# Optimization experiments

Hardware: AMD Instinct MI355X
Metric: run time of the kernel (lower is better)

## Reference

```python
import jax, jax.numpy as jnp
import numpy as np

DIM = 256
RADIUS = 3
DIAM = 2 * RADIUS + 1          # 7
NNEIGH = DIAM * DIAM           # 49
B, H, W = 2, 64, 64
EPS_LN = 1e-6
EPS_NORM = 1e-7


def conv1x1(x, w, b):
    # x: [B,Cin,H,W], w: [Cout,Cin], b: [Cout]
    return jnp.einsum('oi,bihw->bohw', w, x) + b[None, :, None, None]


def layernorm2d(x, g, b):
    # channel-wise norm as in LayerNorm2d (mean/var over channel dim)
    u = x.mean(1, keepdims=True)
    s = ((x - u) ** 2).mean(1, keepdims=True)
    xn = (x - u) / jnp.sqrt(s + EPS_LN)
    return g[None, :, None, None] * xn + b[None, :, None, None]


def unfold_reflect(x, r):
    # torch F.unfold(pad(x, reflect, r), kernel=2r+1).reshape(B,C,D*D,H,W)
    d = 2 * r + 1
    hh, ww = x.shape[2], x.shape[3]
    xp = jnp.pad(x, ((0, 0), (0, 0), (r, r), (r, r)), mode='reflect')
    pats = [xp[:, :, i:i + hh, j:j + ww] for i in range(d) for j in range(d)]
    return jnp.stack(pats, axis=2)  # [B,C,D*D,H,W]


def setup_inputs() -> dict:
    key = jax.random.key(0)
    ks = jax.random.split(key, 20)
    sc_c = 1.0 / np.sqrt(DIM)
    sc_f = 1.0 / np.sqrt(NNEIGH + DIM)
    inp = {
        'spatial_feats': jax.random.normal(ks[0], (B, DIM, H, W), jnp.float32),
        'semantic_feats': jax.random.normal(ks[1], (B, DIM, H, W), jnp.float32),
        # range_proj: conv1x1 -> LN2d -> SiLU -> conv1x1
        'rp_w1': jax.random.normal(ks[2], (DIM, DIM), jnp.float32) * sc_c,
        'rp_b1': jnp.zeros((DIM,), jnp.float32),
        'rp_g': jnp.ones((DIM,), jnp.float32),
        'rp_be': jnp.zeros((DIM,), jnp.float32),
        'rp_w2': jax.random.normal(ks[3], (DIM, DIM), jnp.float32) * sc_c,
        'rp_b2': jnp.zeros((DIM,), jnp.float32),
        # fixup_proj: conv1x1(49+C->49) -> LN2d -> SiLU -> conv1x1(49->49)
        'fp_w1': jax.random.normal(ks[4], (NNEIGH, NNEIGH + DIM), jnp.float32) * sc_f,
        'fp_b1': jnp.zeros((NNEIGH,), jnp.float32),
        'fp_g': jnp.ones((NNEIGH,), jnp.float32),
        'fp_be': jnp.zeros((NNEIGH,), jnp.float32),
        'fp_w2': jax.random.normal(ks[5], (NNEIGH, NNEIGH), jnp.float32) * (1.0 / np.sqrt(NNEIGH)),
        'fp_b2': jnp.zeros((NNEIGH,), jnp.float32),
        # output_proj: conv1x1 -> LN2d -> conv1x1
        'op_w1': jax.random.normal(ks[6], (DIM, DIM), jnp.float32) * sc_c,
        'op_b1': jnp.zeros((DIM,), jnp.float32),
        'op_g': jnp.ones((DIM,), jnp.float32),
        'op_be': jnp.zeros((DIM,), jnp.float32),
        'op_w2': jax.random.normal(ks[7], (DIM, DIM), jnp.float32) * sc_c,
        'op_b2': jnp.zeros((DIM,), jnp.float32),
        'sigma_spatial': jnp.ones((), jnp.float32),
    }
    return inp


def reference(spatial_feats, semantic_feats,
              rp_w1, rp_b1, rp_g, rp_be, rp_w2, rp_b2,
              fp_w1, fp_b1, fp_g, fp_be, fp_w2, fp_b2,
              op_w1, op_b1, op_g, op_be, op_w2, op_b2,
              sigma_spatial):
    scale = jnp.asarray(DIM ** 0.5, spatial_feats.dtype)
    # range_proj(semantic_feats)
    px = conv1x1(semantic_feats, rp_w1, rp_b1)
    px = jax.nn.silu(layernorm2d(px, rp_g, rp_be))
    px = conv1x1(px, rp_w2, rp_b2)  # [B,C,H,W]

    # spatial (Gaussian) kernel over the window
    lin = jnp.linspace(-1.0, 1.0, DIAM)
    xg, yg = jnp.meshgrid(lin, lin, indexing='ij')
    spatial_kernel = jnp.exp(-(xg ** 2 + yg ** 2) / (2.0 * sigma_spatial ** 2))
    spatial_kernel = spatial_kernel.reshape(1, NNEIGH, 1, 1)

    # range kernel: local similarity + softmax over the 49 neighbors
    queries = unfold_reflect(px, RADIUS)                       # [B,C,N,H,W]
    sim = jnp.einsum('bcnhw,bchw->bnhw', queries, px) / scale
    range_kernel = jax.nn.softmax(sim.astype(jnp.float32), axis=1).astype(px.dtype)

    # neighborhoods of spatial features
    neighborhoods = unfold_reflect(spatial_feats, RADIUS)      # [B,C,N,H,W]

    # gated fixup correction
    ck = range_kernel * spatial_kernel                          # [B,N,H,W]
    fx = conv1x1(jnp.concatenate([ck, semantic_feats], axis=1), fp_w1, fp_b1)
    fx = jax.nn.silu(layernorm2d(fx, fp_g, fp_be))
    fx = conv1x1(fx, fp_w2, fp_b2)
    ck = ck + ck * jax.nn.sigmoid(fx)
    ck = ck / (ck.sum(1, keepdims=True) + EPS_NORM)

    # weighted neighborhood sum
    out = jnp.einsum('bcnhw,bnhw->bchw', neighborhoods, ck)

    # output_proj (note: no SiLU here, matching the module)
    out = conv1x1(out, op_w1, op_b1)
    out = layernorm2d(out, op_g, op_be)
    out = conv1x1(out, op_w2, op_b2)
    return out
```

## Files before the change

### kernel.cpp

```cpp
#include <hip/hip_runtime.h>
#include <cstdint>

#define HW 4096
#define C_ 256
#define NN 49
#define KW 305

typedef __bf16 bf16;
typedef bf16 bf16x8 __attribute__((ext_vector_type(8)));
typedef bf16 bf16x4 __attribute__((ext_vector_type(4)));
typedef bf16 bf16x2 __attribute__((ext_vector_type(2)));
typedef float f32x4 __attribute__((ext_vector_type(4)));

#define GLD16(src, dst) __builtin_amdgcn_global_load_lds( \
    (const __attribute__((address_space(1))) uint32_t*)(src), \
    (__attribute__((address_space(3))) uint32_t*)(dst), 16, 0, 0)

__device__ __forceinline__ int refl(int i) { return i < 0 ? -i : (i > 63 ? 126 - i : i); }
__device__ __forceinline__ float sigmoidf_(float x) { return 1.f / (1.f + __expf(-x)); }

__global__ __launch_bounds__(256) void setup_k(const float* __restrict__ spatial,
                                               const float* __restrict__ semantic,
                                               const float* __restrict__ rp_w1,
                                               const float* __restrict__ rp_w2,
                                               const float* __restrict__ op_w1,
                                               const float* __restrict__ op_w2,
                                               const float* __restrict__ fp_w1,
                                               const float* __restrict__ fp_w2,
                                               const float* __restrict__ sigma,
                                               bf16* __restrict__ spb, bf16* __restrict__ seb,
                                               bf16* __restrict__ wrp1, bf16* __restrict__ wrp2,
                                               bf16* __restrict__ wop1, bf16* __restrict__ wop2,
                                               bf16* __restrict__ w1ckb, bf16* __restrict__ w1sb,
                                               bf16* __restrict__ w2Tg, float* __restrict__ sk)
{
    __shared__ float tile[32][33];
    const int bid = blockIdx.x, t = threadIdx.x;
    if (bid < 4096) {
        int z = bid >> 10, r = bid & 1023;
        int b = z & 1;
        const float* src = (z >> 1) ? semantic : spatial;
        bf16* dst = (z >> 1) ? seb : spb;
        int p0 = (r & 127) * 32, c0 = (r >> 7) * 32;
        int tx = t & 31, ty = t >> 5;
        const float* s = src + (size_t)b * C_ * HW;
        #pragma unroll
        for (int i = 0; i < 32; i += 8)
            tile[ty + i][tx] = s[(size_t)(c0 + ty + i) * HW + p0 + tx];
        __syncthreads();
        int p = t >> 3, cq = (t & 7) * 4;
        bf16x4 o = {(bf16)tile[cq][p], (bf16)tile[cq + 1][p], (bf16)tile[cq + 2][p], (bf16)tile[cq + 3][p]};
        *(bf16x4*)&dst[((size_t)b * HW + p0 + p) * C_ + c0 + cq] = o;
        return;
    }
    int pid = bid - 4096;
    if (pid < 256) {
        const float* src = (pid < 64) ? rp_w1 : (pid < 128) ? rp_w2 : (pid < 192) ? op_w1 : op_w2;
        bf16* dst = (pid < 64) ? wrp1 : (pid < 128) ? wrp2 : (pid < 192) ? wop1 : wop2;
        int i = ((pid & 63) * 256 + t) * 4;
        f32x4 v = *(const f32x4*)&src[i];
        bf16x4 o = {(bf16)v[0], (bf16)v[1], (bf16)v[2], (bf16)v[3]};
        *(bf16x4*)&dst[i] = o;
    } else if (pid == 256) {
        if (t < NN) {
            int i = t / 7, j = t % 7;
            float xg = (i - 3) * (1.f / 3.f), yg = (j - 3) * (1.f / 3.f);
            float s = sigma[0];
            sk[t] = __expf(-(xg * xg + yg * yg) / (2.f * s * s));
        }
    } else if (pid < 270) {
        int idx = (pid - 257) * 256 + t;
        if (idx < NN * 64) {
            int k = idx >> 6, o = idx & 63;
            w1ckb[idx] = (o < NN) ? (bf16)fp_w1[o * KW + k] : (bf16)0.f;
        }
    } else if (pid < 334) {
        int idx = (pid - 270) * 256 + t;
        int o = idx >> 8, c = idx & 255;
        w1sb[idx] = (o < NN) ? (bf16)fp_w1[o * KW + NN + c] : (bf16)0.f;
    } else {
        int idx = (pid - 334) * 256 + t;
        if (idx < NN * 64) {
            int k = idx >> 6, o = idx & 63;
            w2Tg[idx] = (o < NN) ? (bf16)fp_w2[o * NN + k] : (bf16)0.f;
        }
    }
}

__device__ __forceinline__ void stage_b(const bf16* __restrict__ Wp, bf16* dst, int kc, int t)
{
    const bf16* gB = Wp + (size_t)(t >> 2) * C_ + kc + (((t & 3) ^ ((t >> 3) & 3)) * 8);
    #pragma unroll
    for (int ii = 0; ii < 4; ++ii)
        GLD16(gB + (size_t)ii * 64 * C_, dst + ii * 2048 + t * 8);
}

template<bool SILU, int MODE>
__global__ __launch_bounds__(256) void conv_pair(const bf16* __restrict__ X,
                                                 const bf16* __restrict__ W1,
                                                 const float* __restrict__ b1v,
                                                 const float* __restrict__ g,
                                                 const float* __restrict__ be,
                                                 const bf16* __restrict__ W2,
                                                 const float* __restrict__ b2v,
                                                 void* __restrict__ Yv)
{
    __shared__ __align__(16) bf16 Xf[32 * 256];
    __shared__ __align__(16) bf16 Mid[32 * 256];
    __shared__ __align__(16) bf16 Bs[2][256 * 32];
    __shared__ float lnred[32][4][2];
    const int t = threadIdx.x;
    const int lane = t & 63, wc = t >> 6;
    const int l15 = lane & 15, kb = lane >> 4;
    const long q0 = (long)blockIdx.x * 32;

    {
        const int r8 = t >> 5, slot = t & 31;
        const bf16* gX = X + (q0 + r8) * C_ + ((slot ^ (r8 & 7)) * 8);
        #pragma unroll
        for (int i = 0; i < 4; ++i)
            GLD16(gX + (size_t)i * 8 * C_, &Xf[i * 2048 + t * 8]);
    }
    stage_b(W1, &Bs[0][0], 0, t);

    const int x7 = l15 & 7;
    const int bsl = (kb ^ ((l15 >> 1) & 3)) * 8;
    int boff[4];
    #pragma unroll
    for (int n = 0; n < 4; ++n)
        boff[n] = (wc * 64 + n * 16 + l15) * 32 + bsl;
    const int a0base = l15 * 256;
    const int a1base = (16 + l15) * 256;

    f32x4 acc[2][4];
    #pragma unroll
    for (int m = 0; m < 2; ++m)
        #pragma unroll
        for (int n = 0; n < 4; ++n) acc[m][n] = (f32x4){0.f, 0.f, 0.f, 0.f};

    __syncthreads();
    int cur = 0;
    #pragma unroll
    for (int ks = 0; ks < 8; ++ks) {
        if (ks < 7) stage_b(W1, &Bs[cur ^ 1][0], (ks + 1) * 32, t);
        const int ko = ((ks * 4 + kb) ^ x7) * 8;
        bf16x8 a0 = *(const bf16x8*)&Xf[a0base + ko];
        bf16x8 a1 = *(const bf16x8*)&Xf[a1base + ko];
        #pragma unroll
        for (int n = 0; n < 4; ++n) {
            bf16x8 b = *(const bf16x8*)&Bs[cur][boff[n]];
            acc[0][n] = __builtin_amdgcn_mfma_f32_16x16x32_bf16(a0, b, acc[0][n], 0, 0, 0);
            acc[1][n] = __builtin_amdgcn_mfma_f32_16x16x32_bf16(a1, b, acc[1][n], 0, 0, 0);
        }
        __syncthreads();
        cur ^= 1;
    }

    stage_b(W2, &Bs[0][0], 0, t);

    float s4[2][4], ss4[2][4];
    #pragma unroll
    for (int m = 0; m < 2; ++m)
        #pragma unroll
        for (int r = 0; r < 4; ++r) { s4[m][r] = 0.f; ss4[m][r] = 0.f; }
    #pragma unroll
    for (int n = 0; n < 4; ++n) {
        float bo = b1v[wc * 64 + n * 16 + l15];
        #pragma unroll
        for (int m = 0; m < 2; ++m)
            #pragma unroll
            for (int r = 0; r < 4; ++r) {
                float v = acc[m][n][r] + bo;
                acc[m][n][r] = v;
                s4[m][r] += v; ss4[m][r] += v * v;
            }
    }
    #pragma unroll
    for (int off = 1; off <= 8; off <<= 1)
        #pragma unroll
        for (int m = 0; m < 2; ++m)
            #pragma unroll
            for (int r = 0; r < 4; ++r) {
                s4[m][r]  += __shfl_xor(s4[m][r], off, 64);
                ss4[m][r] += __shfl_xor(ss4[m][r], off, 64);
            }
    if (l15 == 0) {
        #pragma unroll
        for (int m = 0; m < 2; ++m)
            #pragma unroll
            for (int r = 0; r < 4; ++r) {
                lnred[m * 16 + kb * 4 + r][wc][0] = s4[m][r];
                lnred[m * 16 + kb * 4 + r][wc][1] = ss4[m][r];
            }
    }
    __syncthreads();
    float mean[2][4], rstd[2][4];
    #pragma unroll
    for (int m = 0; m < 2; ++m)
        #pragma unroll
        for (int r = 0; r < 4; ++r) {
            int p = m * 16 + kb * 4 + r;
            float st  = lnred[p][0][0] + lnred[p][1][0] + lnred[p][2][0] + lnred[p][3][0];
            float sst = lnred[p][0][1] + lnred[p][1][1] + lnred[p][2][1] + lnred[p][3][1];
            mean[m][r] = st * (1.f / 256.f);
            float var = sst * (1.f / 256.f) - mean[m][r] * mean[m][r];
            rstd[m][r] = rsqrtf(var + 1e-6f);
        }
    #pragma unroll
    for (int n = 0; n < 4; ++n) {
        int ch = wc * 64 + n * 16 + l15;
        float gv = g[ch], bev = be[ch];
        #pragma unroll
        for (int m = 0; m < 2; ++m)
            #pragma unroll
            for (int r = 0; r < 4; ++r) {
                float y = (acc[m][n][r] - mean[m][r]) * rstd[m][r] * gv + bev;
                if (SILU) y *= sigmoidf_(y);
                int p = m * 16 + kb * 4 + r;
                Mid[p * 256 + (((ch >> 3) ^ (p & 7)) * 8) + (ch & 7)] = (bf16)y;
            }
    }
    __syncthreads();

    f32x4 acc2[2][4];
    #pragma unroll
    for (int m = 0; m < 2; ++m)
        #pragma unroll
        for (int n = 0; n < 4; ++n) acc2[m][n] = (f32x4){0.f, 0.f, 0.f, 0.f};
    cur = 0;
    #pragma unroll
    for (int ks = 0; ks < 8; ++ks) {
        if (ks < 7) stage_b(W2, &Bs[cur ^ 1][0], (ks + 1) * 32, t);
        const int ko = ((ks * 4 + kb) ^ x7) * 8;
        bf16x8 a0 = *(const bf16x8*)&Mid[a0base + ko];
        bf16x8 a1 = *(const bf16x8*)&Mid[a1base + ko];
        #pragma unroll
        for (int n = 0; n < 4; ++n) {
            bf16x8 b = *(const bf16x8*)&Bs[cur][boff[n]];
            acc2[0][n] = __builtin_amdgcn_mfma_f32_16x16x32_bf16(a0, b, acc2[0][n], 0, 0, 0);
            acc2[1][n] = __builtin_amdgcn_mfma_f32_16x16x32_bf16(a1, b, acc2[1][n], 0, 0, 0);
        }
        __syncthreads();
        cur ^= 1;
    }

    if constexpr (MODE == 0) {
        #pragma unroll
        for (int n = 0; n < 4; ++n) {
            int ch = wc * 64 + n * 16 + l15;
            float bo = b2v[ch];
            #pragma unroll
            for (int m = 0; m < 2; ++m)
                #pragma unroll
                for (int r = 0; r < 4; ++r)
                    Xf[(m * 16 + kb * 4 + r) * 256 + ch] = (bf16)(acc2[m][n][r] + bo);
        }
        __syncthreads();
        bf16* Y = (bf16*)Yv;
        const int p = t >> 3, cb = (t & 7) * 32;
        #pragma unroll
        for (int i = 0; i < 4; ++i) {
            bf16x8 v = *(const bf16x8*)&Xf[p * 256 + cb + i * 8];
            *(bf16x8*)&Y[(q0 + p) * C_ + cb + i * 8] = v;
        }
    } else {
        float* Y = (float*)Yv;
        const int bb = (int)(q0 >> 12);
        #pragma unroll
        for (int n = 0; n < 4; ++n) {
            int ch = wc * 64 + n * 16 + l15;
            float bo = b2v[ch];
            #pragma unroll
            for (int m = 0; m < 2; ++m) {
                int pp = (int)(q0 & 4095) + m * 16 + kb * 4;
                f32x4 val = {acc2[m][n][0] + bo, acc2[m][n][1] + bo,
                             acc2[m][n][2] + bo, acc2[m][n][3] + bo};
                *(f32x4*)&Y[((size_t)bb * C_ + ch) * HW + pp] = val;
            }
        }
    }
}

__global__ __launch_bounds__(256) void attn_k(const bf16* __restrict__ px,
                                              const bf16* __restrict__ spb,
                                              const bf16* __restrict__ seb,
                                              const bf16* __restrict__ w1sb,
                                              const bf16* __restrict__ w1ckb,
                                              const bf16* __restrict__ w2Tg,
                                              const float* __restrict__ b1,
                                              const float* __restrict__ b2,
                                              const float* __restrict__ g,
                                              const float* __restrict__ be,
                                              const float* __restrict__ sk,
                                              bf16* __restrict__ outb)
{
    __shared__ __align__(16) bf16 uni[100 * 256];
    __shared__ float S[112 * 17];
    __shared__ float fxs[64 * 17];
    __shared__ __align__(16) bf16 w2lT[NN * 64];
    __shared__ __align__(16) bf16 w1lT[NN * 64];
    __shared__ float ckl[16][64];
    __shared__ float hb[4][64];

    const int t = threadIdx.x, lane = t & 63, wid = t >> 6;
    const int l15 = lane & 15, kb = lane >> 4;
    const int blk = blockIdx.x;
    const int batch = blk >> 8, tt = blk & 255;
    const int h0 = (tt >> 4) * 4, w0 = (tt & 15) * 4;
    const long base = (long)batch * HW;

    const float bo  = (lane < NN) ? b1[lane] : 0.f;
    const float gl  = (lane < NN) ? g[lane] : 0.f;
    const float bel = (lane < NN) ? be[lane] : 0.f;
    const float b2l = (lane < NN) ? b2[lane] : 0.f;
    const float skv = (lane < NN) ? sk[lane] : 0.f;
    const int nn_ = (lane < NN) ? lane : 0;
    const int dy = nn_ / 7, dx = nn_ % 7;

    for (int i = t; i < 392; i += 256) {
        GLD16(w2Tg + (size_t)i * 8, &w2lT[i * 8]);
        GLD16(w1ckb + (size_t)i * 8, &w1lT[i * 8]);
    }

    const int ppy = l15 >> 2, ppx = l15 & 3;
    const long qB = base + (h0 + ppy) * 64 + (w0 + ppx);
    const bf16* bpxp = px + qB * C_ + kb * 8;
    const bf16* bsemp = seb + qB * C_ + kb * 8;

    bool valid[3], ispx[3];
    const bf16* arow[3];
    #pragma unroll
    for (int j = 0; j < 3; ++j) {
        int tid = wid + 4 * j;
        valid[j] = tid < 11;
        ispx[j] = tid < 7;
        int u = tid * 16 + l15;
        int uy = (u * 205) >> 11, ux = u - uy * 10;
        long grow = (u < 100) ? base + refl(h0 + uy - 3) * 64 + refl(w0 + ux - 3) : base;
        int o = ((tid - 7) & 3) * 16 + l15;
        arow[j] = ispx[j] ? (px + grow * C_ + kb * 8)
                          : (w1sb + (size_t)o * C_ + kb * 8);
    }

    f32x4 acc[3];
    #pragma unroll
    for (int j = 0; j < 3; ++j) acc[j] = (f32x4){0.f, 0.f, 0.f, 0.f};

    #pragma unroll
    for (int ks = 0; ks < 8; ++ks) {
        bf16x8 bp = *(const bf16x8*)(bpxp + ks * 32);
        bf16x8 bs = *(const bf16x8*)(bsemp + ks * 32);
        #pragma unroll
        for (int j = 0; j < 3; ++j) {
            if (valid[j]) {
                bf16x8 a = *(const bf16x8*)(arow[j] + ks * 32);
                acc[j] = __builtin_amdgcn_mfma_f32_16x16x32_bf16(a, ispx[j] ? bp : bs, acc[j], 0, 0, 0);
            }
        }
    }
    #pragma unroll
    for (int j = 0; j < 3; ++j) {
        if (valid[j]) {
            int tid = wid + 4 * j;
            float* dst = ispx[j] ? &S[(tid * 16 + kb * 4) * 17 + l15]
                                 : &fxs[(((tid - 7) * 16) + kb * 4) * 17 + l15];
            dst[0] = acc[j][0]; dst[17] = acc[j][1]; dst[34] = acc[j][2]; dst[51] = acc[j][3];
        }
    }
    __syncthreads();

    #pragma unroll
    for (int i = 0; i < 13; ++i) {
        int st = i * 256 + t;
        if (st < 3200) {
            int u = st >> 5, s = st & 31;
            int uy = (u * 205) >> 11, ux = u - uy * 10;
            long grow = base + refl(h0 + uy - 3) * 64 + refl(w0 + ux - 3);
            GLD16(spb + grow * C_ + ((s ^ (u & 7)) * 8), &uni[u * 256 + s * 8]);
        }
    }

    #pragma unroll
    for (int j = 0; j < 4; ++j) {
        int p = wid * 4 + j, py = p >> 2, px4 = p & 3;
        int u = (py + dy) * 10 + px4 + dx;
        float sval = (lane < NN) ? S[u * 17 + p] * 0.0625f : -1e30f;
        float mx = sval;
        #pragma unroll
        for (int off = 32; off; off >>= 1) mx = fmaxf(mx, __shfl_xor(mx, off, 64));
        float ev = (lane < NN) ? __expf(sval - mx) : 0.f;
        float ssum = ev;
        #pragma unroll
        for (int off = 32; off; off >>= 1) ssum += __shfl_xor(ssum, off, 64);
        ckl[p][lane] = (lane < NN) ? (ev / ssum) * skv : 0.f;
    }

    #pragma unroll
    for (int j = 0; j < 4; ++j) {
        int p = wid * 4 + j;
        float fxa = 0.f, fxb = 0.f;
        #pragma unroll
        for (int k = 0; k < 48; k += 2) {
            fxa += (float)w1lT[k * 64 + lane] * ckl[p][k];
            fxb += (float)w1lT[(k + 1) * 64 + lane] * ckl[p][k + 1];
        }
        fxa += (float)w1lT[48 * 64 + lane] * ckl[p][48];
        float fx = fxs[lane * 17 + p] + bo + fxa + fxb;
        float s = fx, ss = fx * fx;
        #pragma unroll
        for (int off = 32; off; off >>= 1) {
            s  += __shfl_xor(s, off, 64);
            ss += __shfl_xor(ss, off, 64);
        }
        float mean = s * (1.f / 49.f);
        float var  = ss * (1.f / 49.f) - mean * mean;
        float rstd = rsqrtf(var + 1e-6f);
        float hv = 0.f;
        if (lane < NN) {
            float xn = (fx - mean) * rstd * gl + bel;
            hv = xn * sigmoidf_(xn);
        }
        hb[wid][lane] = hv;
        float ckv = 0.f;
        if (lane < NN) {
            float ca = 0.f, cb = 0.f;
            #pragma unroll
            for (int k = 0; k < 48; k += 2) {
                ca += (float)w2lT[k * 64 + lane] * hb[wid][k];
                cb += (float)w2lT[(k + 1) * 64 + lane] * hb[wid][k + 1];
            }
            ca += (float)w2lT[48 * 64 + lane] * hb[wid][48];
            ckv = ckl[p][lane] * (1.f + sigmoidf_(b2l + ca + cb));
        }
        float tot = ckv;
        #pragma unroll
        for (int off = 32; off; off >>= 1) tot += __shfl_xor(tot, off, 64);
        ckl[p][lane] = (lane < NN) ? ckv / (tot + 1e-7f) : 0.f;
    }
    __syncthreads();

    const int l31 = lane & 31;
    #pragma unroll
    for (int jj = 0; jj < 2; ++jj) {
        int p = wid * 4 + jj * 2 + (lane >> 5);
        int py = p >> 2, px4 = p & 3;
        long q = base + (h0 + py) * 64 + (w0 + px4);
        int ub = py * 10 + px4;
        float a[8];
        #pragma unroll
        for (int e = 0; e < 8; ++e) a[e] = 0.f;
        for (int dyy = 0; dyy < 7; ++dyy) {
            bf16x8 v[7];
            #pragma unroll
            for (int dxx = 0; dxx < 7; ++dxx) {
                int u = ub + dyy * 10 + dxx;
                v[dxx] = *(const bf16x8*)&uni[u * 256 + ((l31 ^ (u & 7)) * 8)];
            }
            #pragma unroll
            for (int dxx = 0; dxx < 7; ++dxx) {
                float cv = ckl[p][dyy * 7 + dxx];
                #pragma unroll
                for (int e = 0; e < 8; ++e) a[e] += cv * (float)v[dxx][e];
            }
        }
        bf16x8 ov;
        #pragma unroll
        for (int e = 0; e < 8; ++e) ov[e] = (bf16)a[e];
        *(bf16x8*)&outb[q * C_ + l31 * 8] = ov;
    }
}

extern "C" void kernel_launch(void* const* d_in, const int* in_sizes, int n_in,
                              void* d_out, int out_size, void* d_ws, size_t ws_size,
                              hipStream_t stream)
{
    const float* spatial  = (const float*)d_in[0];
    const float* semantic = (const float*)d_in[1];
    const float* rp_w1 = (const float*)d_in[2];
    const float* rp_b1 = (const float*)d_in[3];
    const float* rp_g  = (const float*)d_in[4];
    const float* rp_be = (const float*)d_in[5];
    const float* rp_w2 = (const float*)d_in[6];
    const float* rp_b2 = (const float*)d_in[7];
    const float* fp_w1 = (const float*)d_in[8];
    const float* fp_b1 = (const float*)d_in[9];
    const float* fp_g  = (const float*)d_in[10];
    const float* fp_be = (const float*)d_in[11];
    const float* fp_w2 = (const float*)d_in[12];
    const float* fp_b2 = (const float*)d_in[13];
    const float* op_w1 = (const float*)d_in[14];
    const float* op_b1 = (const float*)d_in[15];
    const float* op_g  = (const float*)d_in[16];
    const float* op_be = (const float*)d_in[17];
    const float* op_w2 = (const float*)d_in[18];
    const float* op_b2 = (const float*)d_in[19];
    const float* sigma = (const float*)d_in[20];

    const size_t NPX = 2 * (size_t)HW;
    float* ws = (float*)d_ws;
    float* sk    = ws;
    bf16* bfbase = (bf16*)(sk + 64);
    bf16* spb = bfbase;
    bf16* seb = spb + NPX * C_;
    bf16* t0  = seb + NPX * C_;
    bf16* t1  = t0  + NPX * C_;
    bf16* wrp1 = t1 + NPX * C_;
    bf16* wrp2 = wrp1 + C_ * C_;
    bf16* wop1 = wrp2 + C_ * C_;
    bf16* wop2 = wop1 + C_ * C_;
    bf16* w1sb = wop2 + C_ * C_;
    bf16* w2Tg = w1sb + 64 * C_;
    bf16* w1ckb = w2Tg + 3200;

    setup_k<<<4443, 256, 0, stream>>>(spatial, semantic, rp_w1, rp_w2, op_w1, op_w2,
                                      fp_w1, fp_w2, sigma,
                                      spb, seb, wrp1, wrp2, wop1, wop2,
                                      w1ckb, w1sb, w2Tg, sk);

    conv_pair<true, 0><<<256, 256, 0, stream>>>(seb, wrp1, rp_b1, rp_g, rp_be, wrp2, rp_b2, t1);

    attn_k<<<512, 256, 0, stream>>>(t1, spb, seb, w1sb, w1ckb, w2Tg, fp_b1, fp_b2,
                                    fp_g, fp_be, sk, t0);

    conv_pair<false, 1><<<256, 256, 0, stream>>>(t0, wop1, op_b1, op_g, op_be, wop2, op_b2, d_out);
}
```

Before: 68.15 us.

## Halve neighborhood LDS tile, stage channels in two halves, keep fixup weights in registers

The attention kernel's spatial-neighborhood LDS buffer is cut from 256 to 128 channels per pixel. The two channel halves are now staged one after the other, with the first half prefetched at kernel start so it overlaps the similarity MFMAs. The fixup conv weights move from LDS into per-lane register arrays, and the ckl row is padded. This shrinks LDS per block (about 51KB down to about 25KB) to allow more resident blocks, at the cost of extra barriers, a second staging pass and about 98 more VGPRs per thread.

New measurement: 66.02 us. -3.1%, faster.

```diff
diff --git a/kernel.cpp b/kernel.cpp
--- a/kernel.cpp
+++ b/kernel.cpp
@@ -294,12 +294,10 @@
                                               const float* __restrict__ sk,
                                               bf16* __restrict__ outb)
 {
-    __shared__ __align__(16) bf16 uni[100 * 256];
+    __shared__ __align__(16) bf16 uni[100 * 128];
     __shared__ float S[112 * 17];
     __shared__ float fxs[64 * 17];
-    __shared__ __align__(16) bf16 w2lT[NN * 64];
-    __shared__ __align__(16) bf16 w1lT[NN * 64];
-    __shared__ float ckl[16][64];
+    __shared__ float ckl[16][65];
     __shared__ float hb[4][64];
 
     const int t = threadIdx.x, lane = t & 63, wid = t >> 6;
@@ -317,10 +315,26 @@
     const int nn_ = (lane < NN) ? lane : 0;
     const int dy = nn_ / 7, dx = nn_ % 7;
 
-    for (int i = t; i < 392; i += 256) {
-        GLD16(w2Tg + (size_t)i * 8, &w2lT[i * 8]);
-        GLD16(w1ckb + (size_t)i * 8, &w1lT[i * 8]);
-    }
+    long sgrow;
+    int sdst;
+    {
+        int st = t;
+        (void)st;
+    }
+#define STAGE_UNI(ci) do { \
+    _Pragma("unroll") \
+    for (int i_ = 0; i_ < 7; ++i_) { \
+        int st_ = i_ * 256 + t; \
+        if (st_ < 1600) { \
+            int u_ = st_ >> 4, s_ = st_ & 15; \
+            int uy_ = (u_ * 205) >> 11, ux_ = u_ - uy_ * 10; \
+            long grow_ = base + refl(h0 + uy_ - 3) * 64 + refl(w0 + ux_ - 3); \
+            GLD16(spb + grow_ * C_ + (ci) * 128 + ((s_ ^ (u_ & 7)) * 8), &uni[u_ * 128 + s_ * 8]); \
+        } \
+    } \
+} while (0)
+
+    STAGE_UNI(0);
 
     const int ppy = l15 >> 2, ppx = l15 & 3;
     const long qB = base + (h0 + ppy) * 64 + (w0 + ppx);
@@ -358,6 +372,14 @@
             }
         }
     }
+
+    float w1r[NN], w2r[NN];
+    #pragma unroll
+    for (int k = 0; k < NN; ++k) {
+        w1r[k] = (float)w1ckb[k * 64 + lane];
+        w2r[k] = (float)w2Tg[k * 64 + lane];
+    }
+
     #pragma unroll
     for (int j = 0; j < 3; ++j) {
         if (valid[j]) {
@@ -370,17 +392,6 @@
     __syncthreads();
 
     #pragma unroll
-    for (int i = 0; i < 13; ++i) {
-        int st = i * 256 + t;
-        if (st < 3200) {
-            int u = st >> 5, s = st & 31;
-            int uy = (u * 205) >> 11, ux = u - uy * 10;
-            long grow = base + refl(h0 + uy - 3) * 64 + refl(w0 + ux - 3);
-            GLD16(spb + grow * C_ + ((s ^ (u & 7)) * 8), &uni[u * 256 + s * 8]);
-        }
-    }
-
-    #pragma unroll
     for (int j = 0; j < 4; ++j) {
         int p = wid * 4 + j, py = p >> 2, px4 = p & 3;
         int u = (py + dy) * 10 + px4 + dx;
@@ -401,10 +412,10 @@
         float fxa = 0.f, fxb = 0.f;
         #pragma unroll
         for (int k = 0; k < 48; k += 2) {
-            fxa += (float)w1lT[k * 64 + lane] * ckl[p][k];
-            fxb += (float)w1lT[(k + 1) * 64 + lane] * ckl[p][k + 1];
-        }
-        fxa += (float)w1lT[48 * 64 + lane] * ckl[p][48];
+            fxa += w1r[k] * ckl[p][k];
+            fxb += w1r[k + 1] * ckl[p][k + 1];
+        }
+        fxa += w1r[48] * ckl[p][48];
         float fx = fxs[lane * 17 + p] + bo + fxa + fxb;
         float s = fx, ss = fx * fx;
         #pragma unroll
@@ -426,10 +437,10 @@
             float ca = 0.f, cb = 0.f;
             #pragma unroll
             for (int k = 0; k < 48; k += 2) {
-                ca += (float)w2lT[k * 64 + lane] * hb[wid][k];
-                cb += (float)w2lT[(k + 1) * 64 + lane] * hb[wid][k + 1];
-            }
-            ca += (float)w2lT[48 * 64 + lane] * hb[wid][48];
+                ca += w2r[k] * hb[wid][k];
+                cb += w2r[k + 1] * hb[wid][k + 1];
+            }
+            ca += w2r[48] * hb[wid][48];
             ckv = ckl[p][lane] * (1.f + sigmoidf_(b2l + ca + cb));
         }
         float tot = ckv;
@@ -439,13 +450,19 @@
     }
     __syncthreads();
 
-    const int l31 = lane & 31;
-    #pragma unroll
-    for (int jj = 0; jj < 2; ++jj) {
-        int p = wid * 4 + jj * 2 + (lane >> 5);
-        int py = p >> 2, px4 = p & 3;
-        long q = base + (h0 + py) * 64 + (w0 + px4);
-        int ub = py * 10 + px4;
+    const int sub = lane >> 4;
+    const int p = wid * 4 + sub;
+    const int py = p >> 2, px4 = p & 3;
+    const long q = base + (h0 + py) * 64 + (w0 + px4);
+    const int ub = py * 10 + px4;
+
+    #pragma unroll
+    for (int ci = 0; ci < 2; ++ci) {
+        if (ci == 1) {
+            __syncthreads();
+            STAGE_UNI(1);
+            __syncthreads();
+        }
         float a[8];
         #pragma unroll
         for (int e = 0; e < 8; ++e) a[e] = 0.f;
@@ -454,7 +471,7 @@
             #pragma unroll
             for (int dxx = 0; dxx < 7; ++dxx) {
                 int u = ub + dyy * 10 + dxx;
-                v[dxx] = *(const bf16x8*)&uni[u * 256 + ((l31 ^ (u & 7)) * 8)];
+                v[dxx] = *(const bf16x8*)&uni[u * 128 + ((l15 ^ (u & 7)) * 8)];
             }
             #pragma unroll
             for (int dxx = 0; dxx < 7; ++dxx) {
@@ -466,8 +483,9 @@
         bf16x8 ov;
         #pragma unroll
         for (int e = 0; e < 8; ++e) ov[e] = (bf16)a[e];
-        *(bf16x8*)&outb[q * C_ + l31 * 8] = ov;
-    }
+        *(bf16x8*)&outb[q * C_ + ci * 128 + l15 * 8] = ov;
+    }
+#undef STAGE_UNI
 }
 
 extern "C" void kernel_launch(void* const* d_in, const int* in_sizes, int n_in,
```
